# Performance work log

Measured on AMD Instinct MI355X. Metric: run time of the kernel, lower is better.

## Reference

```python
import jax, jax.numpy as jnp
import numpy as np

N, S, M = 16, 256, 768
TK, HA = 10, 1          # tK stages, hA heads (from RTM.__init__)
DH = M // HA
EPS = 1e-5
WSCALE = 0.02           # scale on randn weights to keep 10 stacked stages numerically sane


def _pos_bias():
    # bias[i][j][z] = sin(j / 10000**(2z/M)), bias[i][j][z+1] = cos(...); independent of i
    pos = np.arange(S, dtype=np.float64)[:, None]
    z = np.arange(0, M, 2, dtype=np.float64)
    ang = pos / (10000.0 ** (2.0 * z / M))          # (S, M/2)
    pe = np.zeros((S, M), dtype=np.float32)
    pe[:, 0::2] = np.sin(ang)
    pe[:, 1::2] = np.cos(ang)
    return jnp.asarray(pe)

PE = _pos_bias()


def _ln(v, g, b):
    mu = jnp.mean(v, axis=-1, keepdims=True)
    var = jnp.var(v, axis=-1, keepdims=True)
    return (v - mu) / jnp.sqrt(var + EPS) * g + b


def setup_inputs() -> dict:
    key = jax.random.key(0)
    ks = jax.random.split(key, 8)
    rn = lambda k, shp: jax.random.normal(k, shp, dtype=jnp.float32)
    return {
        "x": rn(ks[0], (N, S, M)),
        "weight": rn(ks[1], (M, M)) * WSCALE,
        "Wq": rn(ks[2], (TK, HA, DH, M)) * WSCALE,
        "Wk": rn(ks[3], (TK, HA, DH, M)) * WSCALE,
        "Wv": rn(ks[4], (TK, HA, DH, M)) * WSCALE,
        "Wo": rn(ks[5], (TK, M, M)) * WSCALE,
        "ln1_g": jnp.ones((M,), jnp.float32), "ln1_b": jnp.zeros((M,), jnp.float32),
        "ln2_g": jnp.ones((M,), jnp.float32), "ln2_b": jnp.zeros((M,), jnp.float32),
        "fc1_w": rn(ks[6], (4 * M, M)) * WSCALE, "fc1_b": jnp.zeros((4 * M,), jnp.float32),
        "fc2_w": rn(ks[7], (M, 4 * M)) * WSCALE, "fc2_b": jnp.zeros((M,), jnp.float32),
    }


def reference(x, weight, Wq, Wk, Wv, Wo, ln1_g, ln1_b, ln2_g, ln2_b,
              fc1_w, fc1_b, fc2_w, fc2_b):
    # savespace[i,j] = weight @ x[i,j,:]  (x[j,:,i] after the double transpose), + sin/cos bias
    s0 = jnp.einsum('mn,ijn->ijm', weight, x) + PE[None, :, :]   # (N, S, M)
    inv_sqrt_dh = jnp.float32(1.0 / np.sqrt(DH))

    def mlp(s):
        h = jax.nn.gelu(s @ fc1_w.T + fc1_b, approximate=False)
        return h @ fc2_w.T + fc2_b

    # Sequential over tokens j: token j attends (strictly causal) to the per-stage V
    # of all previous tokens, accumulated in cumV. Within a token, the tK stages run
    # sequentially, each mutating the token's state s (as the torch code mutates savespace).
    def token_step(cumV, s):                # cumV: (TK, N, HA, DH); s: (N, M)
        newV = []
        for a in range(TK):
            sn = _ln(s, ln1_g, ln1_b)
            q = jnp.einsum('hdm,nm->nhd', Wq[a], sn)
            k = jnp.einsum('hdm,nm->nhd', Wk[a], sn)
            v = jnp.einsum('hdm,nm->nhd', Wv[a], sn)
            logit = jnp.sum(q * inv_sqrt_dh * k, axis=-1)                # (N, HA) scalar score
            rsa = jax.nn.softmax(logit[..., None], axis=-1)[..., 0]      # softmax of scalar == 1
            imv = cumV[a]                                                # (N, HA, DH): sum_{subj<j}
            s = jnp.einsum('mk,nk->nm', Wo[a], imv.reshape(N, HA * DH)) + s
            s = _ln(s, ln2_g, ln2_b) + s
            s = mlp(s)
            newV.append(rsa[..., None] * v)
        return cumV + jnp.stack(newV, axis=0), s

    cumV0 = jnp.zeros((TK, N, HA, DH), x.dtype)
    _, ys = jax.lax.scan(token_step, cumV0, jnp.swapaxes(s0, 0, 1))      # ys: (S, N, M)
    return jnp.swapaxes(ys, 0, 1)                                        # (N, S, M)
```

## Files before the change

kernel.cpp:

```cpp
#include <hip/hip_runtime.h>
#include <hip/hip_bf16.h>
#include <math.h>


using bf16   = __bf16;
using bf16x8 = __attribute__((ext_vector_type(8))) __bf16;
using f32x4  = __attribute__((ext_vector_type(4))) float;

#define DEV __device__ __forceinline__

DEV void gload16(const bf16* g, bf16* l) {
  __builtin_amdgcn_global_load_lds(
      (const __attribute__((address_space(1))) unsigned int*)g,
      (__attribute__((address_space(3))) unsigned int*)l, 16, 0, 0);
}

DEV float gelu_f(float x) {
  const float y  = x * 0.70710678118654752f;
  const float ay = fabsf(y);
  const float t  = __builtin_amdgcn_rcpf(__builtin_fmaf(0.3275911f, ay, 1.0f));
  float p = __builtin_fmaf(1.061405429f, t, -1.453152027f);
  p = __builtin_fmaf(p, t, 1.421413741f);
  p = __builtin_fmaf(p, t, -0.284496736f);
  p = __builtin_fmaf(p, t, 0.254829592f);
  p = p * t;
  const float e = __expf(-ay * ay);
  float er = __builtin_fmaf(-p, e, 1.0f);
  er = __builtin_copysignf(er, y);
  return 0.5f * x * (1.0f + er);
}

enum { EPI_PART = 0, EPI_GELU = 1, EPI_B16 = 2 };

template <int BN, int EPI>
__global__ __launch_bounds__(256) void gemm_k(
    const bf16* __restrict__ A, const bf16* __restrict__ B,
    float* __restrict__ outF, bf16* __restrict__ outB,
    const float* __restrict__ aux, int K, int N,
    int kZ, int klen, size_t aZ, size_t bZ, size_t oZ)
{
  constexpr int ABUF = 128 * 32;
  constexpr int BBUF = BN * 32;
  __shared__ bf16 As[2 * ABUF];
  __shared__ bf16 Bs[2 * BBUF];
  const int z = blockIdx.z;
  A += (size_t)z * aZ;
  B += (size_t)z * bZ;
  const int kbeg = z * kZ;
  const int tid  = threadIdx.x;
  const int lane = tid & 63, wave = tid >> 6;
  const int m0 = blockIdx.x * 128, n0 = blockIdx.y * BN;

  const int r  = tid >> 2;
  const int kq = ((tid & 3) - (tid >> 3)) & 3;
  const bf16* aG0 = A + (size_t)(m0 + r) * K + kq * 8 + kbeg;
  const bf16* aG1 = aG0 + (size_t)64 * K;
  const bf16* bG0 = B + (size_t)(n0 + r) * K + kq * 8 + kbeg;
  const bf16* bG1 = bG0 + (size_t)64 * K;

  const int wr = (wave & 1) * 64, wc = (wave >> 1) * (BN / 2);
  const int lr = lane & 15, kb = lane >> 4;
  const int swz  = ((kb + (lr >> 1)) & 3) * 8;
  const int aOff = (wr + lr) * 32 + swz;
  const int bOff = (wc + lr) * 32 + swz;

  constexpr int MT = 4, NT = BN / 32;
  f32x4 acc[MT][NT] = {};
  const int iters = klen >> 5;

  auto stage = [&](int p, int k0) {
    bf16* aD = &As[p * ABUF + tid * 8];
    gload16(aG0 + k0, aD);
    gload16(aG1 + k0, aD + 2048);
    bf16* bD = &Bs[p * BBUF + tid * 8];
    gload16(bG0 + k0, bD);
    if (BN == 128) gload16(bG1 + k0, bD + 2048);
  };

  stage(0, 0);
  for (int it = 0; it < iters; ++it) {
    __syncthreads();
    if (it + 1 < iters) stage((it + 1) & 1, (it + 1) * 32);
    const int pa = (it & 1) * ABUF, pb = (it & 1) * BBUF;
    bf16x8 af[MT], bfv[NT];
#pragma unroll
    for (int t = 0; t < MT; ++t) af[t] = *(const bf16x8*)&As[pa + aOff + t * 512];
#pragma unroll
    for (int t = 0; t < NT; ++t) bfv[t] = *(const bf16x8*)&Bs[pb + bOff + t * 512];
#pragma unroll
    for (int mt = 0; mt < MT; ++mt)
#pragma unroll
      for (int nt = 0; nt < NT; ++nt)
        acc[mt][nt] = __builtin_amdgcn_mfma_f32_16x16x32_bf16(af[mt], bfv[nt], acc[mt][nt], 0, 0, 0);
  }

  const int row0 = m0 + wr + (lane >> 4) * 4;
  const int col0 = n0 + wc + lr;
  float* oF = (EPI == EPI_PART) ? outF + (size_t)z * oZ : nullptr;
  bf16*  oB = (EPI == EPI_B16)  ? outB + (size_t)z * oZ : outB;
#pragma unroll
  for (int mt = 0; mt < MT; ++mt) {
#pragma unroll
    for (int nt = 0; nt < NT; ++nt) {
      const int col = col0 + nt * 16;
      float bias = 0.f;
      if (EPI == EPI_GELU) bias = aux[col];
#pragma unroll
      for (int rg = 0; rg < 4; ++rg) {
        const int row = row0 + mt * 16 + rg;
        float v = acc[mt][nt][rg];
        if (EPI == EPI_PART) {
          oF[(size_t)row * N + col] = v;
        } else if (EPI == EPI_GELU) {
          oB[(size_t)row * N + col] = (bf16)gelu_f(v + bias);
        } else {
          oB[(size_t)row * N + col] = (bf16)v;
        }
      }
    }
  }
}

template <int NP, int MODE>
__global__ __launch_bounds__(256) void reduce_ln(
    const float* __restrict__ P, size_t pZ,
    const float* __restrict__ add, const float* __restrict__ g,
    const float* __restrict__ b, float* __restrict__ Tout,
    bf16* __restrict__ SNout)
{
  const int row = blockIdx.x, t = threadIdx.x;
  float v[3];
#pragma unroll
  for (int c = 0; c < 3; ++c) {
    const int col = t + c * 256;
    float s = P[(size_t)row * 768 + col];
#pragma unroll
    for (int p = 1; p < NP; ++p) s += P[(size_t)p * pZ + (size_t)row * 768 + col];
    if (MODE == 0) s += add[(row & 255) * 768 + col];
    if (MODE == 1) s += add[(size_t)row * 768 + col];
    if (MODE == 2 || MODE == 3) s += add[col];
    v[c] = s;
  }
  if (MODE != 1) {
#pragma unroll
    for (int c = 0; c < 3; ++c) Tout[(size_t)row * 768 + t + c * 256] = v[c];
  }
  if (MODE == 3) return;

  __shared__ float red[8];
  float s = v[0] + v[1] + v[2];
#pragma unroll
  for (int o = 32; o >= 1; o >>= 1) s += __shfl_down(s, o);
  if ((t & 63) == 0) red[t >> 6] = s;
  __syncthreads();
  const float mu = (red[0] + red[1] + red[2] + red[3]) * (1.f / 768.f);
  const float d0 = v[0] - mu, d1 = v[1] - mu, d2 = v[2] - mu;
  float q = d0 * d0 + d1 * d1 + d2 * d2;
#pragma unroll
  for (int o = 32; o >= 1; o >>= 1) q += __shfl_down(q, o);
  if ((t & 63) == 0) red[4 + (t >> 6)] = q;
  __syncthreads();
  const float var = (red[4] + red[5] + red[6] + red[7]) * (1.f / 768.f);
  const float rs = rsqrtf(var + 1e-5f);
  float y0 = d0 * rs * g[t] + b[t];
  float y1 = d1 * rs * g[t + 256] + b[t + 256];
  float y2 = d2 * rs * g[t + 512] + b[t + 512];
  if (MODE == 1) { y0 += v[0]; y1 += v[1]; y2 += v[2]; }
  bf16* o = SNout + (size_t)row * 768;
  o[t] = (bf16)y0; o[t + 256] = (bf16)y1; o[t + 512] = (bf16)y2;
}

__global__ __launch_bounds__(256) void scan_partial_b(
    const bf16* __restrict__ SN, float* __restrict__ Ps)
{
  const int n = blockIdx.x, ch = blockIdx.y, d = blockIdx.z * 256 + threadIdx.x;
  const bf16* base = SN + ((size_t)(n * 256 + ch * 16)) * 768 + d;
  float s = 0.f;
#pragma unroll
  for (int j = 0; j < 16; ++j) s += (float)base[(size_t)j * 768];
  Ps[(size_t)(n * 16 + ch) * 768 + d] = s;
}

__global__ __launch_bounds__(256) void scan_final_b(
    const bf16* __restrict__ SN, const float* __restrict__ Ps,
    bf16* __restrict__ PSb)
{
  const int n = blockIdx.x, ch = blockIdx.y, d = blockIdx.z * 256 + threadIdx.x;
  float run = 0.f;
  for (int c = 0; c < ch; ++c) run += Ps[(size_t)(n * 16 + c) * 768 + d];
  const bf16* vb = SN + ((size_t)(n * 256 + ch * 16)) * 768 + d;
  bf16* ob = PSb + ((size_t)(n * 256 + ch * 16)) * 768 + d;
#pragma unroll
  for (int j = 0; j < 16; ++j) {
    ob[(size_t)j * 768] = (bf16)run;
    run += (float)vb[(size_t)j * 768];
  }
}

__global__ __launch_bounds__(256) void transpose_wv(
    const float* __restrict__ Wv, bf16* __restrict__ WvT)
{
  __shared__ float tile[64][65];
  const int a = blockIdx.z, k0 = blockIdx.x * 64, n0 = blockIdx.y * 64;
  const int c = threadIdx.x & 63, r4 = threadIdx.x >> 6;
  const float* src = Wv + (size_t)a * 589824;
  bf16* dst = WvT + (size_t)a * 589824;
#pragma unroll
  for (int i = 0; i < 16; ++i)
    tile[r4 + i * 4][c] = src[(size_t)(k0 + r4 + i * 4) * 768 + n0 + c];
  __syncthreads();
#pragma unroll
  for (int i = 0; i < 16; ++i) {
    const int n = r4 + i * 4;
    dst[(size_t)(n0 + n) * 768 + k0 + c] = (bf16)tile[c][n];
  }
}

__global__ __launch_bounds__(256) void f32_to_bf16_k(
    const float* __restrict__ in, bf16* __restrict__ out, int n4)
{
  const int i = blockIdx.x * 256 + threadIdx.x;
  if (i >= n4) return;
  const float4 v = ((const float4*)in)[i];
  bf16 h[4] = {(bf16)v.x, (bf16)v.y, (bf16)v.z, (bf16)v.w};
  *(uint2*)(out + 4 * (size_t)i) = *(uint2*)h;
}

__global__ __launch_bounds__(256) void pe_kernel(float* __restrict__ PE)
{
  const int id = blockIdx.x * 256 + threadIdx.x;
  const int j = id / 384, p = id % 384;
  const double ang = (double)j * pow(10000.0, -4.0 * (double)p / 768.0);
  PE[(size_t)j * 768 + 2 * p]     = (float)sin(ang);
  PE[(size_t)j * 768 + 2 * p + 1] = (float)cos(ang);
}

extern "C" void kernel_launch(void* const* d_in, const int* in_sizes, int n_in,
                              void* d_out, int out_size, void* d_ws, size_t ws_size,
                              hipStream_t stream)
{
  const float* x      = (const float*)d_in[0];
  const float* weight = (const float*)d_in[1];
  const float* Wv     = (const float*)d_in[4];
  const float* Wo     = (const float*)d_in[5];
  const float* ln1g   = (const float*)d_in[6];
  const float* ln1b   = (const float*)d_in[7];
  const float* ln2g   = (const float*)d_in[8];
  const float* ln2b   = (const float*)d_in[9];
  const float* fc1w   = (const float*)d_in[10];
  const float* fc1b   = (const float*)d_in[11];
  const float* fc2w   = (const float*)d_in[12];
  const float* fc2b   = (const float*)d_in[13];
  float* out = (float*)d_out;

  char* p = (char*)d_ws;
  auto alloc = [&](size_t bytes) { char* r = p; p += (bytes + 255) & ~(size_t)255; return r; };
  bf16*  Wb_w  = (bf16*)alloc(589824ull * 2);
  bf16*  Wb_o  = (bf16*)alloc(5898240ull * 2);
  bf16*  WvT   = (bf16*)alloc(5898240ull * 2);
  bf16*  Wvo   = (bf16*)alloc(5898240ull * 2);
  bf16*  Wb_f1 = (bf16*)alloc(2359296ull * 2);
  bf16*  Wb_f2 = (bf16*)alloc(2359296ull * 2);
  bf16*  Xb    = (bf16*)alloc(3145728ull * 2);
  float* PEf   = (float*)alloc(196608ull * 4);
  float* T     = (float*)alloc(3145728ull * 4);
  bf16*  SN    = (bf16*)alloc(3145728ull * 2);
  bf16*  PSb   = (bf16*)alloc(3145728ull * 2);
  bf16*  H     = (bf16*)alloc(12582912ull * 2);
  float* Ps    = (float*)alloc(196608ull * 4);
  float* Part  = (float*)alloc(2ull * 3145728ull * 4);

  auto cvt = [&](const float* src, bf16* dst, int n) {
    int n4 = n / 4;
    f32_to_bf16_k<<<(n4 + 255) / 256, 256, 0, stream>>>(src, dst, n4);
  };
  cvt(x, Xb, 3145728);
  cvt(weight, Wb_w, 589824);
  cvt(Wo, Wb_o, 5898240);
  cvt(fc1w, Wb_f1, 2359296);
  cvt(fc2w, Wb_f2, 2359296);
  transpose_wv<<<dim3(12, 12, 10), 256, 0, stream>>>(Wv, WvT);
  pe_kernel<<<384, 256, 0, stream>>>(PEf);

  gemm_k<128, EPI_B16><<<dim3(6, 6, 10), 256, 0, stream>>>(
      Wb_o, WvT, nullptr, Wvo, nullptr, 768, 768, 0, 768, 589824, 589824, 589824);

  gemm_k<64, EPI_PART><<<dim3(32, 12, 2), 256, 0, stream>>>(
      Xb, Wb_w, Part, nullptr, nullptr, 768, 768, 384, 384, 0, 0, 3145728);
  reduce_ln<2, 0><<<4096, 256, 0, stream>>>(Part, 3145728, PEf, ln1g, ln1b, T, SN);

  for (int a = 0; a < 10; ++a) {
    scan_partial_b<<<dim3(16, 16, 3), 256, 0, stream>>>(SN, Ps);
    scan_final_b<<<dim3(16, 16, 3), 256, 0, stream>>>(SN, Ps, PSb);
    gemm_k<64, EPI_PART><<<dim3(32, 12, 2), 256, 0, stream>>>(
        PSb, Wvo + (size_t)a * 589824, Part, nullptr, nullptr, 768, 768, 384, 384, 0, 0, 3145728);
    reduce_ln<2, 1><<<4096, 256, 0, stream>>>(Part, 3145728, T, ln2g, ln2b, nullptr, SN);
    gemm_k<128, EPI_GELU><<<dim3(32, 24, 1), 256, 0, stream>>>(
        SN, Wb_f1, nullptr, H, fc1b, 768, 3072, 0, 768, 0, 0, 0);
    gemm_k<64, EPI_PART><<<dim3(32, 12, 2), 256, 0, stream>>>(
        H, Wb_f2, Part, nullptr, nullptr, 3072, 768, 1536, 1536, 0, 0, 3145728);
    if (a < 9)
      reduce_ln<2, 2><<<4096, 256, 0, stream>>>(Part, 3145728, fc2b, ln1g, ln1b, T, SN);
    else
      reduce_ln<2, 3><<<4096, 256, 0, stream>>>(Part, 3145728, fc2b, nullptr, nullptr, out, nullptr);
  }
  (void)in_sizes; (void)n_in; (void)out_size; (void)ws_size;
}
```

Before: 1.249 ms.

## Add 256x256-tile 8-wave GEMM kernel for MLP fc1/fc2 with XCD-aware remap

Adds a new GEMM kernel with 256x256 output tiles, 512 threads and K-step 64. It interleaves LDS reads, MFMA quarters and staged global-to-LDS loads, uses setprio and remaps block indices across XCDs. The kernel is used for fc1 (with the GELU epilogue) and for fc2, where fc2 now uses split-K 4, so the partial buffer and the reduce_ln split factor grow to 4. The aim is more data reuse and higher MFMA utilisation in the two dominant MLP GEMMs. In exchange the fc1 grid has fewer blocks (192) and the split-K reduction moves more traffic.

```diff
diff --git a/kernel.cpp b/kernel.cpp
--- a/kernel.cpp
+++ b/kernel.cpp
@@ -32,6 +32,150 @@
 
 enum { EPI_PART = 0, EPI_GELU = 1, EPI_B16 = 2 };
 
+#define BARRIER() do { asm volatile("" ::: "memory");                        \
+  __builtin_amdgcn_s_barrier(); asm volatile("" ::: "memory"); } while (0)
+#define LGKM0_FENCE() do {                                                   \
+  asm volatile("s_waitcnt lgkmcnt(0)" ::: "memory");                         \
+  __builtin_amdgcn_sched_barrier(0); } while (0)
+
+template <int EPI>
+__global__ __launch_bounds__(512, 2) void gemm256(
+    const bf16* __restrict__ A, const bf16* __restrict__ B,
+    float* __restrict__ outF, bf16* __restrict__ outB,
+    const float* __restrict__ aux, int K, int N,
+    int kZ, int klen, size_t oZ)
+{
+  __shared__ bf16 As[2][2][8192];
+  __shared__ bf16 Bs[2][2][8192];
+  const int z = blockIdx.z;
+  const int kbeg = z * kZ;
+  const int NT = klen >> 6;
+  const int tid = threadIdx.x, lane = tid & 63, w = tid >> 6;
+  const int wr = w >> 2, wc = w & 3;
+  const int lr = lane & 15, kb = lane >> 4;
+  const int bh = wc >> 1, bcol0 = (wc & 1) * 64;
+  const int rst = tid >> 3, kcst = ((tid & 7) - (tid >> 3)) & 7;
+
+  const int nx = gridDim.x;
+  const int nwg = nx * (int)gridDim.y;
+  int f = blockIdx.x + nx * blockIdx.y;
+  const int xcd = f & 7, idx = f >> 3;
+  const int q8 = nwg >> 3, r8 = nwg & 7;
+  f = (xcd < r8 ? xcd * (q8 + 1) : r8 * (q8 + 1) + (xcd - r8) * q8) + idx;
+  const int m0 = (f % nx) * 256, n0 = (f / nx) * 256;
+
+  const bf16* aG[2] = { A + (size_t)(m0 + rst) * K + kbeg + kcst * 8,
+                        A + (size_t)(m0 + 128 + rst) * K + kbeg + kcst * 8 };
+  const bf16* bG[2] = { B + (size_t)(n0 + rst) * K + kbeg + kcst * 8,
+                        B + (size_t)(n0 + 128 + rst) * K + kbeg + kcst * 8 };
+
+  f32x4 acc[8][4] = {};
+  bf16x8 av[4], bv[8];
+
+  auto stA = [&](int slot, int h, int t) {
+    bf16* d = &As[slot][h][0] + tid * 8;
+    const bf16* g = aG[h] + t * 64;
+    gload16(g, d); gload16(g + (size_t)64 * K, d + 4096);
+  };
+  auto stB = [&](int slot, int h, int t) {
+    bf16* d = &Bs[slot][h][0] + tid * 8;
+    const bf16* g = bG[h] + t * 64;
+    gload16(g, d); gload16(g + (size_t)64 * K, d + 4096);
+  };
+  auto rdA = [&](int s, int q) {
+#pragma unroll
+    for (int j = 0; j < 2; ++j)
+#pragma unroll
+      for (int k = 0; k < 2; ++k) {
+        const int row = (2 * q + j) * 16 + lr;
+        const int p = ((k * 4 + kb) + (lr & 7)) & 7;
+        av[j * 2 + k] = *(const bf16x8*)&As[s][wr][row * 64 + p * 8];
+      }
+  };
+  auto rdB = [&](int s) {
+#pragma unroll
+    for (int nt = 0; nt < 4; ++nt)
+#pragma unroll
+      for (int k = 0; k < 2; ++k) {
+        const int row = bcol0 + nt * 16 + lr;
+        const int p = ((k * 4 + kb) + (lr & 7)) & 7;
+        bv[nt * 2 + k] = *(const bf16x8*)&Bs[s][bh][row * 64 + p * 8];
+      }
+  };
+  auto mfmaQ = [&](int q) {
+    __builtin_amdgcn_s_setprio(1);
+#pragma unroll
+    for (int nt = 0; nt < 4; ++nt)
+#pragma unroll
+      for (int j = 0; j < 2; ++j)
+#pragma unroll
+        for (int k = 0; k < 2; ++k)
+          acc[2 * q + j][nt] = __builtin_amdgcn_mfma_f32_16x16x32_bf16(
+              av[j * 2 + k], bv[nt * 2 + k], acc[2 * q + j][nt], 0, 0, 0);
+    __builtin_amdgcn_s_setprio(0);
+  };
+
+  stA(0, 0, 0); stA(0, 1, 0); stB(0, 0, 0); stB(0, 1, 0);
+  if (NT > 1) { stB(1, 0, 1); stB(1, 1, 1); }
+  if (NT > 1) asm volatile("s_waitcnt vmcnt(4)" ::: "memory");
+  else        asm volatile("s_waitcnt vmcnt(0)" ::: "memory");
+  BARRIER();
+
+  for (int u = 0; u < NT; ++u) {
+    const int s = u & 1;
+    const bool g1 = u + 1 < NT, g2 = u + 2 < NT;
+    rdA(s, 0); rdB(s);
+    if (g1) stA(s ^ 1, 0, u + 1);
+    BARRIER();
+    LGKM0_FENCE();
+    mfmaQ(0);
+    BARRIER();
+    rdA(s, 1);
+    if (g1) stA(s ^ 1, 1, u + 1);
+    BARRIER();
+    LGKM0_FENCE();
+    mfmaQ(1);
+    BARRIER();
+    rdA(s, 2);
+    if (g2) stB(s, 0, u + 2);
+    BARRIER();
+    LGKM0_FENCE();
+    mfmaQ(2);
+    BARRIER();
+    rdA(s, 3);
+    if (g2) stB(s, 1, u + 2);
+    BARRIER();
+    LGKM0_FENCE();
+    mfmaQ(3);
+    if (g2)      asm volatile("s_waitcnt vmcnt(4)" ::: "memory");
+    else if (g1) asm volatile("s_waitcnt vmcnt(0)" ::: "memory");
+    BARRIER();
+  }
+
+  const int row0 = m0 + wr * 128 + (lane >> 4) * 4;
+  const int col0 = n0 + wc * 64 + lr;
+  float* oF = (EPI == EPI_PART) ? outF + (size_t)z * oZ : nullptr;
+#pragma unroll
+  for (int mt = 0; mt < 8; ++mt) {
+#pragma unroll
+    for (int nt = 0; nt < 4; ++nt) {
+      const int col = col0 + nt * 16;
+      float bias = 0.f;
+      if (EPI == EPI_GELU) bias = aux[col];
+#pragma unroll
+      for (int rg = 0; rg < 4; ++rg) {
+        const int row = row0 + mt * 16 + rg;
+        float v = acc[mt][nt][rg];
+        if (EPI == EPI_PART) {
+          oF[(size_t)row * N + col] = v;
+        } else {
+          outB[(size_t)row * N + col] = (bf16)gelu_f(v + bias);
+        }
+      }
+    }
+  }
+}
+
 template <int BN, int EPI>
 __global__ __launch_bounds__(256) void gemm_k(
     const bf16* __restrict__ A, const bf16* __restrict__ B,
@@ -41,8 +185,8 @@
 {
   constexpr int ABUF = 128 * 32;
   constexpr int BBUF = BN * 32;
-  __shared__ bf16 As[2 * ABUF];
-  __shared__ bf16 Bs[2 * BBUF];
+  __shared__ bf16 Asl[2 * ABUF];
+  __shared__ bf16 Bsl[2 * BBUF];
   const int z = blockIdx.z;
   A += (size_t)z * aZ;
   B += (size_t)z * bZ;
@@ -64,15 +208,15 @@
   const int aOff = (wr + lr) * 32 + swz;
   const int bOff = (wc + lr) * 32 + swz;
 
-  constexpr int MT = 4, NT = BN / 32;
-  f32x4 acc[MT][NT] = {};
+  constexpr int MT = 4, NTT = BN / 32;
+  f32x4 acc[MT][NTT] = {};
   const int iters = klen >> 5;
 
   auto stage = [&](int p, int k0) {
-    bf16* aD = &As[p * ABUF + tid * 8];
+    bf16* aD = &Asl[p * ABUF + tid * 8];
     gload16(aG0 + k0, aD);
     gload16(aG1 + k0, aD + 2048);
-    bf16* bD = &Bs[p * BBUF + tid * 8];
+    bf16* bD = &Bsl[p * BBUF + tid * 8];
     gload16(bG0 + k0, bD);
     if (BN == 128) gload16(bG1 + k0, bD + 2048);
   };
@@ -82,15 +226,15 @@
     __syncthreads();
     if (it + 1 < iters) stage((it + 1) & 1, (it + 1) * 32);
     const int pa = (it & 1) * ABUF, pb = (it & 1) * BBUF;
-    bf16x8 af[MT], bfv[NT];
-#pragma unroll
-    for (int t = 0; t < MT; ++t) af[t] = *(const bf16x8*)&As[pa + aOff + t * 512];
-#pragma unroll
-    for (int t = 0; t < NT; ++t) bfv[t] = *(const bf16x8*)&Bs[pb + bOff + t * 512];
+    bf16x8 af[MT], bfv[NTT];
+#pragma unroll
+    for (int t = 0; t < MT; ++t) af[t] = *(const bf16x8*)&Asl[pa + aOff + t * 512];
+#pragma unroll
+    for (int t = 0; t < NTT; ++t) bfv[t] = *(const bf16x8*)&Bsl[pb + bOff + t * 512];
 #pragma unroll
     for (int mt = 0; mt < MT; ++mt)
 #pragma unroll
-      for (int nt = 0; nt < NT; ++nt)
+      for (int nt = 0; nt < NTT; ++nt)
         acc[mt][nt] = __builtin_amdgcn_mfma_f32_16x16x32_bf16(af[mt], bfv[nt], acc[mt][nt], 0, 0, 0);
   }
 
@@ -101,7 +245,7 @@
 #pragma unroll
   for (int mt = 0; mt < MT; ++mt) {
 #pragma unroll
-    for (int nt = 0; nt < NT; ++nt) {
+    for (int nt = 0; nt < NTT; ++nt) {
       const int col = col0 + nt * 16;
       float bias = 0.f;
       if (EPI == EPI_GELU) bias = aux[col];
@@ -268,7 +412,7 @@
   bf16*  PSb   = (bf16*)alloc(3145728ull * 2);
   bf16*  H     = (bf16*)alloc(12582912ull * 2);
   float* Ps    = (float*)alloc(196608ull * 4);
-  float* Part  = (float*)alloc(2ull * 3145728ull * 4);
+  float* Part  = (float*)alloc(4ull * 3145728ull * 4);
 
   auto cvt = [&](const float* src, bf16* dst, int n) {
     int n4 = n / 4;
@@ -295,14 +439,14 @@
     gemm_k<64, EPI_PART><<<dim3(32, 12, 2), 256, 0, stream>>>(
         PSb, Wvo + (size_t)a * 589824, Part, nullptr, nullptr, 768, 768, 384, 384, 0, 0, 3145728);
     reduce_ln<2, 1><<<4096, 256, 0, stream>>>(Part, 3145728, T, ln2g, ln2b, nullptr, SN);
-    gemm_k<128, EPI_GELU><<<dim3(32, 24, 1), 256, 0, stream>>>(
-        SN, Wb_f1, nullptr, H, fc1b, 768, 3072, 0, 768, 0, 0, 0);
-    gemm_k<64, EPI_PART><<<dim3(32, 12, 2), 256, 0, stream>>>(
-        H, Wb_f2, Part, nullptr, nullptr, 3072, 768, 1536, 1536, 0, 0, 3145728);
+    gemm256<EPI_GELU><<<dim3(16, 12, 1), 512, 0, stream>>>(
+        SN, Wb_f1, nullptr, H, fc1b, 768, 3072, 0, 768, 0);
+    gemm256<EPI_PART><<<dim3(16, 3, 4), 512, 0, stream>>>(
+        H, Wb_f2, Part, nullptr, nullptr, 3072, 768, 768, 768, 3145728);
     if (a < 9)
-      reduce_ln<2, 2><<<4096, 256, 0, stream>>>(Part, 3145728, fc2b, ln1g, ln1b, T, SN);
+      reduce_ln<4, 2><<<4096, 256, 0, stream>>>(Part, 3145728, fc2b, ln1g, ln1b, T, SN);
     else
-      reduce_ln<2, 3><<<4096, 256, 0, stream>>>(Part, 3145728, fc2b, nullptr, nullptr, out, nullptr);
+      reduce_ln<4, 3><<<4096, 256, 0, stream>>>(Part, 3145728, fc2b, nullptr, nullptr, out, nullptr);
   }
   (void)in_sizes; (void)n_in; (void)out_size; (void)ws_size;
 }
```

Result: slower. 1.291 ms (+3.3%).
